# Optimization experiments

Measured on AMD Instinct MI355X. Metric: run time of the kernel, lower is better.

## Reference

```python
import jax, jax.numpy as jnp
import numpy as np

IN_CH = 256
OUT_CH = 256
LATENT = 512
SCALE = 1.0 / IN_CH ** 0.5


def setup_inputs() -> dict:
    key = jax.random.key(0)
    k1, k2, k3, k4 = jax.random.split(key, 4)
    return {
        "x": jax.random.normal(k1, (16, IN_CH, 64, 64), dtype=jnp.float32),
        "w": jax.random.normal(k2, (16, LATENT), dtype=jnp.float32),
        "style_w": jax.random.normal(k3, (IN_CH, LATENT), dtype=jnp.float32) * (1.0 / LATENT ** 0.5),
        "style_b": jnp.zeros((IN_CH,), dtype=jnp.float32),
        "weight": jax.random.normal(k4, (1, OUT_CH, IN_CH, 3, 3), dtype=jnp.float32),
    }


def reference(x, w, style_w, style_b, weight):
    b, c, h, ws = x.shape
    # style = Linear(latent -> in_channels), reshaped to [b,1,in,1,1]
    style = (w @ style_w.T + style_b)[:, None, :, None, None]
    wt = weight * SCALE                    # [1, O, I, 3, 3]
    wt = wt * (style + 1.0)                # [b, O, I, 3, 3]
    demod = jax.lax.rsqrt(jnp.sum(wt * wt, axis=(2, 3, 4), keepdims=True) + 1e-8)
    wt = wt * demod
    # grouped conv: fold batch into channels, groups = b
    x2 = x.reshape(1, b * c, h, ws)
    k = wt.reshape(b * OUT_CH, c, 3, 3)
    out = jax.lax.conv_general_dilated(
        x2, k,
        window_strides=(1, 1),
        padding=((1, 1), (1, 1)),
        dimension_numbers=("NCHW", "OIHW", "NCHW"),
        feature_group_count=b,
    )
    return out.reshape(b, OUT_CH, h, ws)
```

## Files before the change

kernel.cpp:

```cpp
#include <hip/hip_runtime.h>
#include <hip/hip_bf16.h>

#define IN_CH 256
#define OUT_CH 256
#define LATENT 512
#define MSCALE (1.0f / 16.0f)

typedef __attribute__((ext_vector_type(8)))  short bf16x8;
typedef __attribute__((ext_vector_type(16))) float f32x16;
typedef unsigned short u16;

__device__ __forceinline__ u16 f2bf(float f) {
  unsigned int x = __float_as_uint(f);
  x += 0x7fffu + ((x >> 16) & 1u);
  return (u16)(x >> 16);
}

__device__ __forceinline__ void gload_lds16(const u16* g, u16* l) {
#if defined(__has_builtin) && __has_builtin(__builtin_amdgcn_global_load_lds)
  __builtin_amdgcn_global_load_lds(
      (const __attribute__((address_space(1))) unsigned int*)g,
      (__attribute__((address_space(3))) unsigned int*)l, 16, 0, 0);
#else
  int lane = __builtin_amdgcn_mbcnt_hi(~0u, __builtin_amdgcn_mbcnt_lo(~0u, 0));
  ((uint4*)l)[lane] = *(const uint4*)g;
#endif
}

__global__ void k_style(const float* __restrict__ w, const float* __restrict__ sw,
                        const float* __restrict__ sb, float* __restrict__ mod) {
  __shared__ float ws[LATENT];
  const int b = blockIdx.x, tid = threadIdx.x;
  ws[tid] = w[b * LATENT + tid];
  ws[tid + 256] = w[b * LATENT + 256 + tid];
  __syncthreads();
  const float4* sr = (const float4*)(sw + (size_t)tid * LATENT);
  const float4* wr = (const float4*)ws;
  float s = 0.f;
#pragma unroll 8
  for (int l = 0; l < LATENT / 4; ++l) {
    float4 a = sr[l], c = wr[l];
    s += a.x * c.x + a.y * c.y + a.z * c.z + a.w * c.w;
  }
  mod[b * IN_CH + tid] = (1.0f + s + sb[tid]) * MSCALE;
}

__global__ void k_wsq(const float* __restrict__ weight, float* __restrict__ wsq,
                      u16* __restrict__ wb) {
  const int o = blockIdx.x, i = threadIdx.x;
  const float* wp = weight + ((size_t)o * IN_CH + i) * 9;
  float s = 0.f;
#pragma unroll
  for (int t = 0; t < 9; ++t) {
    float v = wp[t];
    s += v * v;
    wb[((size_t)t * OUT_CH + o) * IN_CH + i] = f2bf(v);
  }
  wsq[o * IN_CH + i] = s;
}

__global__ void k_demod(const float* __restrict__ mod, const float* __restrict__ wsq,
                        float* __restrict__ demod) {
  __shared__ float m2[IN_CH];
  const int b = blockIdx.x, tid = threadIdx.x;
  float m = mod[b * IN_CH + tid];
  m2[tid] = m * m;
  __syncthreads();
  float s = 1e-8f;
  const float* wr = wsq + (size_t)tid * IN_CH;
#pragma unroll 4
  for (int i = 0; i < IN_CH; ++i) s += m2[i] * wr[i];
  demod[b * OUT_CH + tid] = rsqrtf(s);
}

__global__ void k_pad(const float* __restrict__ x, const float* __restrict__ mod,
                      u16* __restrict__ xs) {
  const int bid = blockIdx.x;
  const int b = bid / 66, pr = bid - b * 66;
  const int i = threadIdx.x;
  u16* row = xs + (size_t)((b * 66 + pr) * 66) * IN_CH;
  if (pr == 0 || pr == 65) {
    for (int c = 0; c < 66; ++c) row[c * IN_CH + i] = 0;
  } else {
    const float ms = mod[b * IN_CH + i];
    const float* xp = x + (size_t)((b * IN_CH + i) * 64 + (pr - 1)) * 64;
    row[i] = 0;
    row[65 * IN_CH + i] = 0;
#pragma unroll 4
    for (int c = 0; c < 64; ++c) row[(c + 1) * IN_CH + i] = f2bf(xp[c] * ms);
  }
}

__global__ __launch_bounds__(256, 2)
void k_conv(const u16* __restrict__ xs, const u16* __restrict__ wb,
            const float* __restrict__ demod, float* __restrict__ out) {
  __shared__ __align__(16) u16 xlds[10 * 66 * 32];
  __shared__ __align__(16) u16 wlds[9 * 64 * 32];

  const int tid = threadIdx.x;
  const int lane = tid & 63;
  const int wid = tid >> 6;
  const int ol = lane & 31;
  const int hi = lane >> 5;
  const int aswz = (ol >> 1) & 3;

  const int bid = blockIdx.x;
  const int sbid = ((bid & 7) << 6) | (bid >> 3);
  const int otile = (sbid & 3) << 6;
  const int hbase = ((sbid >> 2) & 7) << 3;
  const int b = sbid >> 5;

  f32x16 acc[2][4] = {};

  const u16* xsb = xs + (size_t)((b * 66 + hbase) * 66) * IN_CH;

  for (int ic = 0; ic < 8; ++ic) {
    const int ibase = ic * 32;
    __syncthreads();

#pragma unroll
    for (int it = 0; it < 10; ++it) {
      int q = it * 256 + tid;
      int cq = q >> 2, s = q & 3;
      int c = cq % 66;
      int g = s ^ ((c >> 1) & 3);
      gload_lds16(xsb + (size_t)cq * IN_CH + ibase + g * 8,
                  xlds + (size_t)(it * 256 + wid * 64) * 8);
    }
    if (tid < 80) {
      int q = 2560 + tid;
      int cq = q >> 2, s = q & 3;
      int c = cq % 66;
      int g = s ^ ((c >> 1) & 3);
      gload_lds16(xsb + (size_t)cq * IN_CH + ibase + g * 8,
                  xlds + (size_t)(2560 + wid * 64) * 8);
    }
#pragma unroll
    for (int it = 0; it < 9; ++it) {
      int q = it * 256 + tid;
      int cell = q >> 2, s = q & 3;
      int o = cell & 63;
      int g = s ^ ((o >> 1) & 3);
      gload_lds16(wb + (size_t)((cell >> 6) * 256 + otile + o) * IN_CH + ibase + g * 8,
                  wlds + (size_t)(it * 256 + wid * 64) * 8);
    }
    __syncthreads();

#pragma unroll
    for (int t = 0; t < 9; ++t) {
      const int dh = t / 3;
      const int dw = t - dh * 3;
#pragma unroll
      for (int k = 0; k < 2; ++k) {
        const int g = 2 * k + hi;
        bf16x8 a0 = *(const bf16x8*)(wlds + (size_t)((t * 64 + ol) * 4 + (g ^ aswz)) * 8);
        bf16x8 a1 = *(const bf16x8*)(wlds + (size_t)((t * 64 + 32 + ol) * 4 + (g ^ aswz)) * 8);
#pragma unroll
        for (int ps = 0; ps < 4; ++ps) {
          const int r = 2 * wid + (ps >> 1) + dh;
          const int c = (ps & 1) * 32 + ol + dw;
          bf16x8 bf = *(const bf16x8*)(xlds + (size_t)((r * 66 + c) * 4 + (g ^ ((c >> 1) & 3))) * 8);
          acc[0][ps] = __builtin_amdgcn_mfma_f32_32x32x16_bf16(a0, bf, acc[0][ps], 0, 0, 0);
          acc[1][ps] = __builtin_amdgcn_mfma_f32_32x32x16_bf16(a1, bf, acc[1][ps], 0, 0, 0);
        }
      }
    }
  }

  const float* dmb = demod + b * OUT_CH + otile;
  float* outb = out + (size_t)b * OUT_CH * 4096;
#pragma unroll
  for (int os = 0; os < 2; ++os) {
    float dm[16];
#pragma unroll
    for (int qd = 0; qd < 4; ++qd) {
      float4 d4 = *(const float4*)(dmb + os * 32 + qd * 8 + hi * 4);
      dm[qd * 4 + 0] = d4.x; dm[qd * 4 + 1] = d4.y;
      dm[qd * 4 + 2] = d4.z; dm[qd * 4 + 3] = d4.w;
    }
#pragma unroll
    for (int ps = 0; ps < 4; ++ps) {
      const int prow = hbase + 2 * wid + (ps >> 1);
      const int col = (ps & 1) * 32 + ol;
#pragma unroll
      for (int rr = 0; rr < 16; ++rr) {
        const int orow = (rr & 3) + 8 * (rr >> 2) + 4 * hi;
        const int o = otile + os * 32 + orow;
        outb[(size_t)o * 4096 + prow * 64 + col] = acc[os][ps][rr] * dm[rr];
      }
    }
  }
}

extern "C" void kernel_launch(void* const* d_in, const int* in_sizes, int n_in,
                              void* d_out, int out_size, void* d_ws, size_t ws_size,
                              hipStream_t stream) {
  const float* x  = (const float*)d_in[0];
  const float* w  = (const float*)d_in[1];
  const float* sw = (const float*)d_in[2];
  const float* sb = (const float*)d_in[3];
  const float* wt = (const float*)d_in[4];
  float* out = (float*)d_out;

  char* ws = (char*)d_ws;
  u16*   xs    = (u16*)(ws);
  u16*   wb    = (u16*)(ws + 35684352);
  float* mod   = (float*)(ws + 36864000);
  float* demod = (float*)(ws + 36880384);
  float* wsq   = (float*)(ws + 36896768);
  if (ws_size < 37158912u) return;

  k_style<<<16, 256, 0, stream>>>(w, sw, sb, mod);
  k_wsq  <<<256, 256, 0, stream>>>(wt, wsq, wb);
  k_demod<<<16, 256, 0, stream>>>(mod, wsq, demod);
  k_pad  <<<16 * 66, 256, 0, stream>>>(x, mod, xs);
  k_conv <<<512, 256, 0, stream>>>(xs, wb, demod, out);
}
```

Baseline: 123.4 us.

## Double-buffer conv LDS staging with 16-channel chunks, fuse style and demod kernels

The conv main loop now uses two LDS buffers of 16 input channels each, issuing the next chunk's global-to-LDS loads before computing the current one. This removes the per-iteration load/compute serialisation and one barrier, and adds setprio around the MFMA block. Precomputed load offsets replace the XOR swizzle with a split-half layout, which may bring LDS bank conflicts back. The style and demod kernels are merged into one, which drops a launch, and k_pad reads x as float4.

```diff
diff --git a/kernel.cpp b/kernel.cpp
--- a/kernel.cpp
+++ b/kernel.cpp
@@ -27,9 +27,11 @@
 #endif
 }
 
-__global__ void k_style(const float* __restrict__ w, const float* __restrict__ sw,
-                        const float* __restrict__ sb, float* __restrict__ mod) {
+__global__ void k_style_demod(const float* __restrict__ w, const float* __restrict__ sw,
+                              const float* __restrict__ sb, const float* __restrict__ wsq,
+                              float* __restrict__ mod, float* __restrict__ demod) {
   __shared__ float ws[LATENT];
+  __shared__ float m2[IN_CH];
   const int b = blockIdx.x, tid = threadIdx.x;
   ws[tid] = w[b * LATENT + tid];
   ws[tid + 256] = w[b * LATENT + 256 + tid];
@@ -42,7 +44,15 @@
     float4 a = sr[l], c = wr[l];
     s += a.x * c.x + a.y * c.y + a.z * c.z + a.w * c.w;
   }
-  mod[b * IN_CH + tid] = (1.0f + s + sb[tid]) * MSCALE;
+  float m = (1.0f + s + sb[tid]) * MSCALE;
+  mod[b * IN_CH + tid] = m;
+  m2[tid] = m * m;
+  __syncthreads();
+  float acc = 1e-8f;
+  const float* q = wsq + (size_t)tid * IN_CH;
+#pragma unroll 4
+  for (int i = 0; i < IN_CH; ++i) acc += m2[i] * q[i];
+  demod[b * OUT_CH + tid] = rsqrtf(acc);
 }
 
 __global__ void k_wsq(const float* __restrict__ weight, float* __restrict__ wsq,
@@ -57,20 +67,6 @@
     wb[((size_t)t * OUT_CH + o) * IN_CH + i] = f2bf(v);
   }
   wsq[o * IN_CH + i] = s;
-}
-
-__global__ void k_demod(const float* __restrict__ mod, const float* __restrict__ wsq,
-                        float* __restrict__ demod) {
-  __shared__ float m2[IN_CH];
-  const int b = blockIdx.x, tid = threadIdx.x;
-  float m = mod[b * IN_CH + tid];
-  m2[tid] = m * m;
-  __syncthreads();
-  float s = 1e-8f;
-  const float* wr = wsq + (size_t)tid * IN_CH;
-#pragma unroll 4
-  for (int i = 0; i < IN_CH; ++i) s += m2[i] * wr[i];
-  demod[b * OUT_CH + tid] = rsqrtf(s);
 }
 
 __global__ void k_pad(const float* __restrict__ x, const float* __restrict__ mod,
@@ -83,26 +79,31 @@
     for (int c = 0; c < 66; ++c) row[c * IN_CH + i] = 0;
   } else {
     const float ms = mod[b * IN_CH + i];
-    const float* xp = x + (size_t)((b * IN_CH + i) * 64 + (pr - 1)) * 64;
+    const float4* xp = (const float4*)(x + (size_t)((b * IN_CH + i) * 64 + (pr - 1)) * 64);
     row[i] = 0;
     row[65 * IN_CH + i] = 0;
-#pragma unroll 4
-    for (int c = 0; c < 64; ++c) row[(c + 1) * IN_CH + i] = f2bf(xp[c] * ms);
+#pragma unroll
+    for (int c4 = 0; c4 < 16; ++c4) {
+      float4 v = xp[c4];
+      row[(c4 * 4 + 1) * IN_CH + i] = f2bf(v.x * ms);
+      row[(c4 * 4 + 2) * IN_CH + i] = f2bf(v.y * ms);
+      row[(c4 * 4 + 3) * IN_CH + i] = f2bf(v.z * ms);
+      row[(c4 * 4 + 4) * IN_CH + i] = f2bf(v.w * ms);
+    }
   }
 }
 
 __global__ __launch_bounds__(256, 2)
 void k_conv(const u16* __restrict__ xs, const u16* __restrict__ wb,
             const float* __restrict__ demod, float* __restrict__ out) {
-  __shared__ __align__(16) u16 xlds[10 * 66 * 32];
-  __shared__ __align__(16) u16 wlds[9 * 64 * 32];
+  __shared__ __align__(16) u16 xlds[2 * 10 * 2 * 66 * 8];
+  __shared__ __align__(16) u16 wlds[2 * 9 * 2 * 64 * 8];
 
   const int tid = threadIdx.x;
   const int lane = tid & 63;
   const int wid = tid >> 6;
   const int ol = lane & 31;
   const int hi = lane >> 5;
-  const int aswz = (ol >> 1) & 3;
 
   const int bid = blockIdx.x;
   const int sbid = ((bid & 7) << 6) | (bid >> 3);
@@ -110,61 +111,70 @@
   const int hbase = ((sbid >> 2) & 7) << 3;
   const int b = sbid >> 5;
 
+  const u16* xsb = xs + (size_t)((b * 66 + hbase) * 66) * IN_CH;
+
+  int xoff[5];
+#pragma unroll
+  for (int it = 0; it < 5; ++it) {
+    int p = it * 256 + tid;
+    int r = p / 132, rem = p - r * 132;
+    int g = rem / 66, c = rem - g * 66;
+    xoff[it] = (r * 66 + c) * IN_CH + g * 8;
+  }
+  const int xofft = (9 * 66 + 26 + tid) * IN_CH + 8;
+  int woff[4];
+#pragma unroll
+  for (int it = 0; it < 4; ++it) {
+    int p = it * 256 + tid;
+    int t = p >> 7, g = (p >> 6) & 1, o = p & 63;
+    woff[it] = (t * OUT_CH + otile + o) * IN_CH + g * 8;
+  }
+  const int wofft = (8 * OUT_CH + otile + (tid & 63)) * IN_CH + ((tid >> 6) & 1) * 8;
+
+  auto stage = [&](int buf, int ic) {
+    const int ib = ic * 16;
+    u16* xd = xlds + buf * 10560;
+#pragma unroll
+    for (int it = 0; it < 5; ++it)
+      gload_lds16(xsb + xoff[it] + ib, xd + (size_t)(it * 256 + wid * 64) * 8);
+    if (tid < 40)
+      gload_lds16(xsb + xofft + ib, xd + (size_t)(1280 + wid * 64) * 8);
+    u16* wd = wlds + buf * 9216;
+#pragma unroll
+    for (int it = 0; it < 4; ++it)
+      gload_lds16(wb + woff[it] + ib, wd + (size_t)(it * 256 + wid * 64) * 8);
+    if (tid < 128)
+      gload_lds16(wb + wofft + ib, wd + (size_t)(1024 + wid * 64) * 8);
+  };
+
   f32x16 acc[2][4] = {};
 
-  const u16* xsb = xs + (size_t)((b * 66 + hbase) * 66) * IN_CH;
-
-  for (int ic = 0; ic < 8; ++ic) {
-    const int ibase = ic * 32;
+  stage(0, 0);
+  __syncthreads();
+
+#pragma unroll 2
+  for (int ic = 0; ic < 16; ++ic) {
+    const int buf = ic & 1;
+    if (ic < 15) stage(buf ^ 1, ic + 1);
+    const u16* xp = xlds + buf * 10560;
+    const u16* wp = wlds + buf * 9216;
+    __builtin_amdgcn_s_setprio(1);
+#pragma unroll
+    for (int t = 0; t < 9; ++t) {
+      const int dh = t / 3, dw = t - dh * 3;
+      bf16x8 a0 = *(const bf16x8*)(wp + (size_t)((t * 2 + hi) * 64 + ol) * 8);
+      bf16x8 a1 = *(const bf16x8*)(wp + (size_t)((t * 2 + hi) * 64 + 32 + ol) * 8);
+#pragma unroll
+      for (int ps = 0; ps < 4; ++ps) {
+        const int r = 2 * wid + (ps >> 1) + dh;
+        const int c = (ps & 1) * 32 + ol + dw;
+        bf16x8 bf = *(const bf16x8*)(xp + (size_t)((r * 2 + hi) * 66 + c) * 8);
+        acc[0][ps] = __builtin_amdgcn_mfma_f32_32x32x16_bf16(a0, bf, acc[0][ps], 0, 0, 0);
+        acc[1][ps] = __builtin_amdgcn_mfma_f32_32x32x16_bf16(a1, bf, acc[1][ps], 0, 0, 0);
+      }
+    }
+    __builtin_amdgcn_s_setprio(0);
     __syncthreads();
-
-#pragma unroll
-    for (int it = 0; it < 10; ++it) {
-      int q = it * 256 + tid;
-      int cq = q >> 2, s = q & 3;
-      int c = cq % 66;
-      int g = s ^ ((c >> 1) & 3);
-      gload_lds16(xsb + (size_t)cq * IN_CH + ibase + g * 8,
-                  xlds + (size_t)(it * 256 + wid * 64) * 8);
-    }
-    if (tid < 80) {
-      int q = 2560 + tid;
-      int cq = q >> 2, s = q & 3;
-      int c = cq % 66;
-      int g = s ^ ((c >> 1) & 3);
-      gload_lds16(xsb + (size_t)cq * IN_CH + ibase + g * 8,
-                  xlds + (size_t)(2560 + wid * 64) * 8);
-    }
-#pragma unroll
-    for (int it = 0; it < 9; ++it) {
-      int q = it * 256 + tid;
-      int cell = q >> 2, s = q & 3;
-      int o = cell & 63;
-      int g = s ^ ((o >> 1) & 3);
-      gload_lds16(wb + (size_t)((cell >> 6) * 256 + otile + o) * IN_CH + ibase + g * 8,
-                  wlds + (size_t)(it * 256 + wid * 64) * 8);
-    }
-    __syncthreads();
-
-#pragma unroll
-    for (int t = 0; t < 9; ++t) {
-      const int dh = t / 3;
-      const int dw = t - dh * 3;
-#pragma unroll
-      for (int k = 0; k < 2; ++k) {
-        const int g = 2 * k + hi;
-        bf16x8 a0 = *(const bf16x8*)(wlds + (size_t)((t * 64 + ol) * 4 + (g ^ aswz)) * 8);
-        bf16x8 a1 = *(const bf16x8*)(wlds + (size_t)((t * 64 + 32 + ol) * 4 + (g ^ aswz)) * 8);
-#pragma unroll
-        for (int ps = 0; ps < 4; ++ps) {
-          const int r = 2 * wid + (ps >> 1) + dh;
-          const int c = (ps & 1) * 32 + ol + dw;
-          bf16x8 bf = *(const bf16x8*)(xlds + (size_t)((r * 66 + c) * 4 + (g ^ ((c >> 1) & 3))) * 8);
-          acc[0][ps] = __builtin_amdgcn_mfma_f32_32x32x16_bf16(a0, bf, acc[0][ps], 0, 0, 0);
-          acc[1][ps] = __builtin_amdgcn_mfma_f32_32x32x16_bf16(a1, bf, acc[1][ps], 0, 0, 0);
-        }
-      }
-    }
   }
 
   const float* dmb = demod + b * OUT_CH + otile;
@@ -210,9 +220,8 @@
   float* wsq   = (float*)(ws + 36896768);
   if (ws_size < 37158912u) return;
 
-  k_style<<<16, 256, 0, stream>>>(w, sw, sb, mod);
-  k_wsq  <<<256, 256, 0, stream>>>(wt, wsq, wb);
-  k_demod<<<16, 256, 0, stream>>>(mod, wsq, demod);
-  k_pad  <<<16 * 66, 256, 0, stream>>>(x, mod, xs);
-  k_conv <<<512, 256, 0, stream>>>(xs, wb, demod, out);
-}
+  k_wsq        <<<256, 256, 0, stream>>>(wt, wsq, wb);
+  k_style_demod<<<16, 256, 0, stream>>>(w, sw, sb, wsq, mod, demod);
+  k_pad        <<<16 * 66, 256, 0, stream>>>(x, mod, xs);
+  k_conv       <<<512, 256, 0, stream>>>(xs, wb, demod, out);
+}
```

After: 132.5 us. 1.07x slower.
